# Kernel tuning notes

Hardware: AMD Instinct MI355X
Metric: run time of the kernel (lower is better)

Reference implementation:

```python
import jax, jax.numpy as jnp
import numpy as np


def setup_inputs() -> dict:
    key = jax.random.key(0)
    ks = jax.random.split(key, 6)
    B, E, N, F = 512, 4, 256, 64
    node = jax.random.normal(ks[0], (B, N, F), dtype=jnp.float32)
    adj = jax.random.uniform(ks[1], (B, E, N, N), dtype=jnp.float32)
    s = 1.0 / np.sqrt(F)
    W_edge = jax.random.uniform(ks[2], (E, F, F), dtype=jnp.float32, minval=-s, maxval=s)
    b_edge = jax.random.uniform(ks[3], (E, F), dtype=jnp.float32, minval=-s, maxval=s)
    W_add = jax.random.uniform(ks[4], (F, F), dtype=jnp.float32, minval=-s, maxval=s)
    b_add = jax.random.uniform(ks[5], (F,), dtype=jnp.float32, minval=-s, maxval=s)
    return {"node": node, "adj": adj, "W_edge": W_edge, "b_edge": b_edge,
            "W_add": W_add, "b_add": b_add}


def reference(node, adj, W_edge, b_edge, W_add, b_add):
    # per-edge-type linear: [B,N,F_in] x [E,F_in,F_out] -> [B,E,N,F_out]
    hidden = jnp.einsum('bnf,efg->beng', node, W_edge) + b_edge[None, :, None, :]
    # adjacency-weighted aggregation per edge type: [B,E,N,N] @ [B,E,N,F_out]
    msg = jnp.einsum('benm,bemg->beng', adj, hidden)
    # sum over edge types + residual linear (dropout=0, activation=None)
    out = jnp.sum(msg, axis=1) + node @ W_add + b_add
    return out
```

## Files before the change

kernel.cpp:

```cpp
#include <hip/hip_runtime.h>

typedef __attribute__((ext_vector_type(8))) short short8;
typedef __attribute__((ext_vector_type(4))) float f32x4;

#define MFMA16(a, b, c) __builtin_amdgcn_mfma_f32_16x16x32_bf16((a), (b), (c), 0, 0, 0)

static __device__ inline short f2bf(float x) {
    union { float f; unsigned u; } v;
    v.f = x;
    unsigned r = v.u + 0x7fffu + ((v.u >> 16) & 1u);
    return (short)(r >> 16);
}
static __device__ inline short4 f2bf4(float4 v) {
    short4 s;
    s.x = f2bf(v.x); s.y = f2bf(v.y); s.z = f2bf(v.z); s.w = f2bf(v.w);
    return s;
}

__global__ __launch_bounds__(256, 2) void gconv_kernel(
    const float* __restrict__ node,
    const float* __restrict__ adj,
    const float* __restrict__ W_edge,
    const float* __restrict__ b_edge,
    const float* __restrict__ W_add,
    const float* __restrict__ b_add,
    float* __restrict__ out)
{
    constexpr int E = 4;

    __shared__ short adjL[256][72];
    __shared__ short hiddenT[64][264];
    __shared__ short wT[64][72];
    const int b    = blockIdx.x;
    const int t    = threadIdx.x;
    const int lane = t & 63;
    const int w    = t >> 6;
    const int col  = lane & 15;
    const int kq   = lane >> 4;

    const float* nodeB = node + (size_t)b * (256 * 64);
    short8 anode[4][2];
    #pragma unroll
    for (int rt = 0; rt < 4; ++rt)
        #pragma unroll
        for (int h = 0; h < 2; ++h) {
            const float* p = nodeB + (64 * w + 16 * rt + col) * 64 + 32 * h + 8 * kq;
            float4 v0 = *(const float4*)p;
            float4 v1 = *(const float4*)(p + 4);
            short8 a;
            a[0] = f2bf(v0.x); a[1] = f2bf(v0.y); a[2] = f2bf(v0.z); a[3] = f2bf(v0.w);
            a[4] = f2bf(v1.x); a[5] = f2bf(v1.y); a[6] = f2bf(v1.z); a[7] = f2bf(v1.w);
            anode[rt][h] = a;
        }

    #pragma unroll
    for (int i = 0; i < 16; ++i) {
        int idx = i * 256 + t;
        wT[idx & 63][idx >> 6] = f2bf(W_add[idx]);
    }
    __syncthreads();

    f32x4 acc[4][4];
    {
        const f32x4 zf = {0.f, 0.f, 0.f, 0.f};
        #pragma unroll
        for (int rt = 0; rt < 4; ++rt)
            #pragma unroll
            for (int ct = 0; ct < 4; ++ct)
                acc[rt][ct] = zf;
        #pragma unroll
        for (int h = 0; h < 2; ++h) {
            short8 bfr[4];
            #pragma unroll
            for (int ct = 0; ct < 4; ++ct)
                bfr[ct] = *(const short8*)&wT[16 * ct + col][32 * h + 8 * kq];
            #pragma unroll
            for (int rt = 0; rt < 4; ++rt)
                #pragma unroll
                for (int ct = 0; ct < 4; ++ct)
                    acc[rt][ct] = MFMA16(anode[rt][h], bfr[ct], acc[rt][ct]);
        }
    }
    __syncthreads();

    for (int e = 0; e < E; ++e) {
        const float* We = W_edge + e * (64 * 64);
        #pragma unroll
        for (int i = 0; i < 16; ++i) {
            int idx = i * 256 + t;
            wT[idx & 63][idx >> 6] = f2bf(We[idx]);
        }
        __syncthreads();

        #pragma unroll
        for (int rt = 0; rt < 4; ++rt) {
            #pragma unroll
            for (int ct = 0; ct < 4; ++ct) {
                short8 b0 = *(const short8*)&wT[16 * ct + col][8 * kq];
                short8 b1 = *(const short8*)&wT[16 * ct + col][32 + 8 * kq];
                f32x4 h = {0.f, 0.f, 0.f, 0.f};
                h = MFMA16(anode[rt][0], b0, h);
                h = MFMA16(anode[rt][1], b1, h);
                float bias = b_edge[e * 64 + 16 * ct + col];
                short4 s;
                s.x = f2bf(h.x + bias); s.y = f2bf(h.y + bias);
                s.z = f2bf(h.z + bias); s.w = f2bf(h.w + bias);
                *(short4*)&hiddenT[16 * ct + col][64 * w + 16 * rt + 4 * kq] = s;
            }
        }
        __syncthreads();

        const float* adjE = adj + ((size_t)(b * 4 + e)) * (256 * 256);
        for (int kt = 0; kt < 4; ++kt) {
            {
                const int c4  = t & 15;
                const int r0  = t >> 4;
                const float* base = adjE + kt * 64 + c4 * 4;
                #pragma unroll
                for (int i = 0; i < 16; ++i) {
                    int row = i * 16 + r0;
                    float4 v = *(const float4*)(base + row * 256);
                    *(short4*)&adjL[row][c4 * 4] = f2bf4(v);
                }
            }
            __syncthreads();

            #pragma unroll
            for (int ks2 = 0; ks2 < 2; ++ks2) {
                short8 afrag[4], bfrag[4];
                #pragma unroll
                for (int rt = 0; rt < 4; ++rt)
                    afrag[rt] = *(const short8*)&adjL[64 * w + 16 * rt + col][32 * ks2 + 8 * kq];
                #pragma unroll
                for (int ct = 0; ct < 4; ++ct)
                    bfrag[ct] = *(const short8*)&hiddenT[16 * ct + col][kt * 64 + 32 * ks2 + 8 * kq];
                #pragma unroll
                for (int rt = 0; rt < 4; ++rt)
                    #pragma unroll
                    for (int ct = 0; ct < 4; ++ct)
                        acc[rt][ct] = MFMA16(afrag[rt], bfrag[ct], acc[rt][ct]);
            }
            __syncthreads();
        }
    }

    float* outB = out + (size_t)b * (256 * 64);
    #pragma unroll
    for (int ct = 0; ct < 4; ++ct) {
        float bias = b_add[16 * ct + col];
        #pragma unroll
        for (int rt = 0; rt < 4; ++rt) {
            int row = 64 * w + 16 * rt + 4 * kq;
            #pragma unroll
            for (int r = 0; r < 4; ++r)
                outB[(size_t)(row + r) * 64 + 16 * ct + col] = acc[rt][ct][r] + bias;
        }
    }
}

extern "C" void kernel_launch(void* const* d_in, const int* in_sizes, int n_in,
                              void* d_out, int out_size, void* d_ws, size_t ws_size,
                              hipStream_t stream) {
    const float* node   = (const float*)d_in[0];
    const float* adj    = (const float*)d_in[1];
    const float* W_edge = (const float*)d_in[2];
    const float* b_edge = (const float*)d_in[3];
    const float* W_add  = (const float*)d_in[4];
    const float* b_add  = (const float*)d_in[5];
    float* out = (float*)d_out;

    gconv_kernel<<<dim3(512), dim3(256), 0, stream>>>(
        node, adj, W_edge, b_edge, W_add, b_add, out);
}
```

Baseline: 712.5 us.

## Split each batch across two blocks and stream adj directly into MFMA registers

The grid doubles so each block owns half of the output rows of one batch element. Each block still recomputes the full hidden matrix, so that work is duplicated. The adjacency tile is no longer staged through LDS: each wave loads its A-fragments from global memory straight into registers, converts to bf16, and prefetches the next k-slice, which removes the adjL buffer and the per-tile barriers. Launch bounds rise to 3 blocks per CU to use the freed LDS and registers, at the cost of the duplicated hidden computation and less coalesced row-strided adj loads.

Result: slower. 779.7 us (+9.4%).

```diff
diff --git a/kernel.cpp b/kernel.cpp
--- a/kernel.cpp
+++ b/kernel.cpp
@@ -11,13 +11,15 @@
     unsigned r = v.u + 0x7fffu + ((v.u >> 16) & 1u);
     return (short)(r >> 16);
 }
-static __device__ inline short4 f2bf4(float4 v) {
-    short4 s;
-    s.x = f2bf(v.x); s.y = f2bf(v.y); s.z = f2bf(v.z); s.w = f2bf(v.w);
-    return s;
+
+static __device__ inline short8 pack_frag(float4 v0, float4 v1) {
+    short8 a;
+    a[0] = f2bf(v0.x); a[1] = f2bf(v0.y); a[2] = f2bf(v0.z); a[3] = f2bf(v0.w);
+    a[4] = f2bf(v1.x); a[5] = f2bf(v1.y); a[6] = f2bf(v1.z); a[7] = f2bf(v1.w);
+    return a;
 }
 
-__global__ __launch_bounds__(256, 2) void gconv_kernel(
+__global__ __launch_bounds__(256, 3) void gconv_kernel(
     const float* __restrict__ node,
     const float* __restrict__ adj,
     const float* __restrict__ W_edge,
@@ -26,12 +28,12 @@
     const float* __restrict__ b_add,
     float* __restrict__ out)
 {
-    constexpr int E = 4;
-
-    __shared__ short adjL[256][72];
     __shared__ short hiddenT[64][264];
     __shared__ short wT[64][72];
-    const int b    = blockIdx.x;
+
+    const int bb   = blockIdx.x;
+    const int b    = bb >> 1;
+    const int mh   = bb & 1;
     const int t    = threadIdx.x;
     const int lane = t & 63;
     const int w    = t >> 6;
@@ -39,18 +41,23 @@
     const int kq   = lane >> 4;
 
     const float* nodeB = node + (size_t)b * (256 * 64);
+
     short8 anode[4][2];
     #pragma unroll
     for (int rt = 0; rt < 4; ++rt)
         #pragma unroll
         for (int h = 0; h < 2; ++h) {
             const float* p = nodeB + (64 * w + 16 * rt + col) * 64 + 32 * h + 8 * kq;
-            float4 v0 = *(const float4*)p;
-            float4 v1 = *(const float4*)(p + 4);
-            short8 a;
-            a[0] = f2bf(v0.x); a[1] = f2bf(v0.y); a[2] = f2bf(v0.z); a[3] = f2bf(v0.w);
-            a[4] = f2bf(v1.x); a[5] = f2bf(v1.y); a[6] = f2bf(v1.z); a[7] = f2bf(v1.w);
-            anode[rt][h] = a;
+            anode[rt][h] = pack_frag(*(const float4*)p, *(const float4*)(p + 4));
+        }
+
+    short8 ares[2][2];
+    #pragma unroll
+    for (int rt = 0; rt < 2; ++rt)
+        #pragma unroll
+        for (int h = 0; h < 2; ++h) {
+            const float* p = nodeB + (128 * mh + 32 * w + 16 * rt + col) * 64 + 32 * h + 8 * kq;
+            ares[rt][h] = pack_frag(*(const float4*)p, *(const float4*)(p + 4));
         }
 
     #pragma unroll
@@ -60,11 +67,11 @@
     }
     __syncthreads();
 
-    f32x4 acc[4][4];
+    f32x4 acc[2][4];
     {
         const f32x4 zf = {0.f, 0.f, 0.f, 0.f};
         #pragma unroll
-        for (int rt = 0; rt < 4; ++rt)
+        for (int rt = 0; rt < 2; ++rt)
             #pragma unroll
             for (int ct = 0; ct < 4; ++ct)
                 acc[rt][ct] = zf;
@@ -75,15 +82,15 @@
             for (int ct = 0; ct < 4; ++ct)
                 bfr[ct] = *(const short8*)&wT[16 * ct + col][32 * h + 8 * kq];
             #pragma unroll
-            for (int rt = 0; rt < 4; ++rt)
+            for (int rt = 0; rt < 2; ++rt)
                 #pragma unroll
                 for (int ct = 0; ct < 4; ++ct)
-                    acc[rt][ct] = MFMA16(anode[rt][h], bfr[ct], acc[rt][ct]);
+                    acc[rt][ct] = MFMA16(ares[rt][h], bfr[ct], acc[rt][ct]);
         }
     }
     __syncthreads();
 
-    for (int e = 0; e < E; ++e) {
+    for (int e = 0; e < 4; ++e) {
         const float* We = W_edge + e * (64 * 64);
         #pragma unroll
         for (int i = 0; i < 16; ++i) {
@@ -110,38 +117,43 @@
         }
         __syncthreads();
 
-        const float* adjE = adj + ((size_t)(b * 4 + e)) * (256 * 256);
-        for (int kt = 0; kt < 4; ++kt) {
-            {
-                const int c4  = t & 15;
-                const int r0  = t >> 4;
-                const float* base = adjE + kt * 64 + c4 * 4;
+        const float* adjE = adj + ((size_t)(b * 4 + e)) * (256 * 256)
+                                + (size_t)(128 * mh) * 256;
+        float4 cur[2][2], nxt[2][2];
+        #pragma unroll
+        for (int rt = 0; rt < 2; ++rt) {
+            const float* p = adjE + (32 * w + 16 * rt + col) * 256 + 8 * kq;
+            cur[rt][0] = *(const float4*)p;
+            cur[rt][1] = *(const float4*)(p + 4);
+        }
+        for (int ks = 0; ks < 8; ++ks) {
+            if (ks < 7) {
                 #pragma unroll
-                for (int i = 0; i < 16; ++i) {
-                    int row = i * 16 + r0;
-                    float4 v = *(const float4*)(base + row * 256);
-                    *(short4*)&adjL[row][c4 * 4] = f2bf4(v);
+                for (int rt = 0; rt < 2; ++rt) {
+                    const float* p = adjE + (32 * w + 16 * rt + col) * 256
+                                   + (ks + 1) * 32 + 8 * kq;
+                    nxt[rt][0] = *(const float4*)p;
+                    nxt[rt][1] = *(const float4*)(p + 4);
                 }
             }
-            __syncthreads();
-
+            short8 bfrag[4];
             #pragma unroll
-            for (int ks2 = 0; ks2 < 2; ++ks2) {
-                short8 afrag[4], bfrag[4];
-                #pragma unroll
-                for (int rt = 0; rt < 4; ++rt)
-                    afrag[rt] = *(const short8*)&adjL[64 * w + 16 * rt + col][32 * ks2 + 8 * kq];
+            for (int ct = 0; ct < 4; ++ct)
+                bfrag[ct] = *(const short8*)&hiddenT[16 * ct + col][ks * 32 + 8 * kq];
+            #pragma unroll
+            for (int rt = 0; rt < 2; ++rt) {
+                short8 a = pack_frag(cur[rt][0], cur[rt][1]);
                 #pragma unroll
                 for (int ct = 0; ct < 4; ++ct)
-                    bfrag[ct] = *(const short8*)&hiddenT[16 * ct + col][kt * 64 + 32 * ks2 + 8 * kq];
-                #pragma unroll
-                for (int rt = 0; rt < 4; ++rt)
-                    #pragma unroll
-                    for (int ct = 0; ct < 4; ++ct)
-                        acc[rt][ct] = MFMA16(afrag[rt], bfrag[ct], acc[rt][ct]);
+                    acc[rt][ct] = MFMA16(a, bfrag[ct], acc[rt][ct]);
             }
-            __syncthreads();
+            #pragma unroll
+            for (int rt = 0; rt < 2; ++rt) {
+                cur[rt][0] = nxt[rt][0];
+                cur[rt][1] = nxt[rt][1];
+            }
         }
+        __syncthreads();
     }
 
     float* outB = out + (size_t)b * (256 * 64);
@@ -149,8 +161,8 @@
     for (int ct = 0; ct < 4; ++ct) {
         float bias = b_add[16 * ct + col];
         #pragma unroll
-        for (int rt = 0; rt < 4; ++rt) {
-            int row = 64 * w + 16 * rt + 4 * kq;
+        for (int rt = 0; rt < 2; ++rt) {
+            int row = 128 * mh + 32 * w + 16 * rt + 4 * kq;
             #pragma unroll
             for (int r = 0; r < 4; ++r)
                 outB[(size_t)(row + r) * 64 + 16 * ct + col] = acc[rt][ct][r] + bias;
@@ -169,6 +181,6 @@
     const float* b_add  = (const float*)d_in[5];
     float* out = (float*)d_out;
 
-    gconv_kernel<<<dim3(512), dim3(256), 0, stream>>>(
+    gconv_kernel<<<dim3(1024), dim3(256), 0, stream>>>(
         node, adj, W_edge, b_edge, W_add, b_add, out);
 }
```
